# Kernel tuning notes

Hardware: AMD Instinct MI355X
Metric: run time of the kernel (lower is better)

## Reference

```python
import jax, jax.numpy as jnp
import numpy as np


def setup_inputs() -> dict:
    key = jax.random.key(0)
    k1, k2 = jax.random.split(key)
    B, T, D = 16, 512, 384
    x = jax.random.normal(k1, (B, T, D), dtype=jnp.float32)
    durations = jax.random.randint(k2, (B, T), 0, 8, dtype=jnp.int64)
    return {"x": x, "durations": durations, "max_len": 4096}


def reference(x, durations, max_len):
    # x: [B, T, D], durations: [B, T] int, max_len: static int
    # Each phoneme t is repeated durations[b, t] times along the frame axis,
    # then sequences are zero-padded to a common length.
    cum = jnp.cumsum(durations, axis=1)              # [B, T] exclusive upper bounds
    frames = jnp.arange(max_len)                     # [F]
    # frame f belongs to phoneme idx where cum[idx-1] <= f < cum[idx]
    idx = jax.vmap(lambda c: jnp.searchsorted(c, frames, side="right"))(cum)  # [B, F]
    valid = frames[None, :] < cum[:, -1][:, None]    # [B, F] frames past total -> pad
    idx = jnp.minimum(idx, durations.shape[1] - 1)   # clamp out-of-range gather
    out = jnp.take_along_axis(x, idx[:, :, None], axis=1)  # [B, F, D]
    return jnp.where(valid[:, :, None], out, jnp.zeros((), dtype=x.dtype))
```

## Files before the change

### kernel.cpp

```cpp
#include <hip/hip_runtime.h>

#define BB   16
#define TT   512
#define FF   4096
#define DD4  96
#define FPT  16
#define TILES (FF / FPT)
#define NTHR 256

__global__ __launch_bounds__(TT) void build_idx_kernel(
    const int* __restrict__ dur, int* __restrict__ fidx) {
    const int b = blockIdx.x;
    const int t = threadIdx.x;
    int* fb = fidx + b * FF;

#pragma unroll
    for (int k = 0; k < FF / TT; ++k) fb[k * TT + t] = -1;

    __shared__ int s[TT];
    const int d = dur[b * TT + t];
    s[t] = d;
    __syncthreads();
#pragma unroll
    for (int off = 1; off < TT; off <<= 1) {
        int v = (t >= off) ? s[t - off] : 0;
        __syncthreads();
        s[t] += v;
        __syncthreads();
    }
    const int cum = s[t];
    const int start = cum - d;
    const int end = cum < FF ? cum : FF;
    for (int f = start; f < end; ++f) fb[f] = t;
}

__global__ __launch_bounds__(NTHR) void gather_kernel(
    const float4* __restrict__ x, const int* __restrict__ fidx,
    float4* __restrict__ out) {
    const int bid  = blockIdx.x;
    const int b    = bid / TILES;
    const int tile = bid - b * TILES;
    const int t    = threadIdx.x;
    const int fl   = t >> 4;
    const int c0   = t & 15;
    const int f    = tile * FPT + fl;

    const int idx = fidx[b * FF + f];
    float4* dst = out + ((size_t)b * FF + f) * DD4;

    if (idx >= 0) {
        const float4* src = x + ((size_t)b * TT + idx) * DD4;
#pragma unroll
        for (int k = 0; k < 6; ++k) dst[c0 + 16 * k] = src[c0 + 16 * k];
    } else {
        const float4 z = make_float4(0.f, 0.f, 0.f, 0.f);
#pragma unroll
        for (int k = 0; k < 6; ++k) dst[c0 + 16 * k] = z;
    }
}

extern "C" void kernel_launch(void* const* d_in, const int* in_sizes, int n_in,
                              void* d_out, int out_size, void* d_ws, size_t ws_size,
                              hipStream_t stream) {
    const float* x = (const float*)d_in[0];
    const int* dur = (const int*)d_in[1];
    int* fidx = (int*)d_ws;

    build_idx_kernel<<<BB, TT, 0, stream>>>(dur, fidx);
    gather_kernel<<<BB * TILES, NTHR, 0, stream>>>(
        (const float4*)x, fidx, (float4*)d_out);
}
```

Measured before the change: 118.5 us.

## Use wave-shuffle scan, XCD-aware block remap, and nontemporal output stores

New measurement: 124.1 us. 4.7% more time.

```diff
diff --git a/kernel.cpp b/kernel.cpp
--- a/kernel.cpp
+++ b/kernel.cpp
@@ -7,6 +7,9 @@
 #define FPT  16
 #define TILES (FF / FPT)
 #define NTHR 256
+#define NXCD 8
+
+typedef float f4 __attribute__((ext_vector_type(4)));
 
 __global__ __launch_bounds__(TT) void build_idx_kernel(
     const int* __restrict__ dur, int* __restrict__ fidx) {
@@ -17,27 +20,37 @@
 #pragma unroll
     for (int k = 0; k < FF / TT; ++k) fb[k * TT + t] = -1;
 
-    __shared__ int s[TT];
     const int d = dur[b * TT + t];
-    s[t] = d;
+
+    int v = d;
+#pragma unroll
+    for (int off = 1; off < 64; off <<= 1) {
+        int u = __shfl_up(v, off, 64);
+        if ((t & 63) >= off) v += u;
+    }
+
+    __shared__ int wsum[TT / 64];
+    const int wid = t >> 6;
+    if ((t & 63) == 63) wsum[wid] = v;
     __syncthreads();
+
+    int base = 0;
 #pragma unroll
-    for (int off = 1; off < TT; off <<= 1) {
-        int v = (t >= off) ? s[t - off] : 0;
-        __syncthreads();
-        s[t] += v;
-        __syncthreads();
-    }
-    const int cum = s[t];
+    for (int w = 0; w < TT / 64 - 1; ++w)
+        if (w < wid) base += wsum[w];
+
+    const int cum = v + base;
     const int start = cum - d;
     const int end = cum < FF ? cum : FF;
     for (int f = start; f < end; ++f) fb[f] = t;
 }
 
 __global__ __launch_bounds__(NTHR) void gather_kernel(
-    const float4* __restrict__ x, const int* __restrict__ fidx,
-    float4* __restrict__ out) {
-    const int bid  = blockIdx.x;
+    const f4* __restrict__ x, const int* __restrict__ fidx,
+    f4* __restrict__ out) {
+    int bid = blockIdx.x;
+    bid = (bid & (NXCD - 1)) * (BB * TILES / NXCD) + (bid >> 3);
+
     const int b    = bid / TILES;
     const int tile = bid - b * TILES;
     const int t    = threadIdx.x;
@@ -46,16 +59,20 @@
     const int f    = tile * FPT + fl;
 
     const int idx = fidx[b * FF + f];
-    float4* dst = out + ((size_t)b * FF + f) * DD4;
+    f4* dst = out + ((size_t)b * FF + f) * DD4;
 
     if (idx >= 0) {
-        const float4* src = x + ((size_t)b * TT + idx) * DD4;
+        const f4* src = x + ((size_t)b * TT + idx) * DD4;
 #pragma unroll
-        for (int k = 0; k < 6; ++k) dst[c0 + 16 * k] = src[c0 + 16 * k];
+        for (int k = 0; k < 6; ++k) {
+            f4 v = src[c0 + 16 * k];
+            __builtin_nontemporal_store(v, &dst[c0 + 16 * k]);
+        }
     } else {
-        const float4 z = make_float4(0.f, 0.f, 0.f, 0.f);
+        const f4 z = {0.f, 0.f, 0.f, 0.f};
 #pragma unroll
-        for (int k = 0; k < 6; ++k) dst[c0 + 16 * k] = z;
+        for (int k = 0; k < 6; ++k)
+            __builtin_nontemporal_store(z, &dst[c0 + 16 * k]);
     }
 }
 
@@ -68,5 +85,5 @@
 
     build_idx_kernel<<<BB, TT, 0, stream>>>(dur, fidx);
     gather_kernel<<<BB * TILES, NTHR, 0, stream>>>(
-        (const float4*)x, fidx, (float4*)d_out);
+        (const f4*)x, fidx, (f4*)d_out);
 }
```
